# Performance work log

Measured on AMD Instinct MI355X. Metric: run time of the kernel, lower is better.

Reference implementation:

```python
import jax, jax.numpy as jnp
import numpy as np

INF = 1.0e15  # matches the TF module's 1e15 additive mask constant


def setup_inputs() -> dict:
    key = jax.random.key(0)
    kq, kk, kv, kp = jax.random.split(key, 4)
    B, S, D = 8, 4096, 64
    q = jax.random.normal(kq, (B, S, D), dtype=jnp.float32)
    k = jax.random.normal(kk, (B, S, D), dtype=jnp.float32)
    v = jax.random.normal(kv, (B, S, D), dtype=jnp.float32)
    # binary key-padding mask: 1 = masked. Broadcasts over seq_q.
    pad_mask = jax.random.randint(kp, (B, 1, S), 0, 2).astype(jnp.float32)
    # causal look-ahead mask: 1 above the diagonal (future positions masked)
    look_ahead_mask = (1.0 - jnp.tril(jnp.ones((S, S), dtype=jnp.float32)))
    return {"q": q, "k": k, "v": v, "pad_mask": pad_mask,
            "look_ahead_mask": look_ahead_mask}


def reference(q, k, v, pad_mask, look_ahead_mask):
    d_model = jnp.asarray(q.shape[2], dtype=q.dtype)
    # (B, Sq, Sk) score matrix, scaled
    score_logits = jnp.einsum("bqd,bkd->bqk", q, k) / jnp.sqrt(d_model)
    score_logits = score_logits + pad_mask * (-INF)          # broadcast (B,1,Sk)
    score_logits = score_logits + look_ahead_mask * (-INF)   # broadcast (Sq,Sk)
    attention_weight = jax.nn.softmax(score_logits, axis=-1)
    context_vector = jnp.einsum("bqk,bkd->bqd", attention_weight, v)
    return context_vector, attention_weight
```

## Files before the change

kernel.cpp:

```cpp
#include <hip/hip_runtime.h>

#define S_LEN 4096
#define D_DIM 64
#define NEG_BIG 1.0e15f
#define NC1 8
#define SSTAT (8 * 64 * NC1 * 64)
#define NPAD_OFF SSTAT
#define WS_FLOATS_NEEDED (NPAD_OFF + 16)
#define VSTRIDE 70

typedef __bf16 bf16_t;
typedef bf16_t bf16x8 __attribute__((ext_vector_type(8)));
typedef bf16_t bf16x4v __attribute__((ext_vector_type(4)));
typedef bf16_t bf16x2v __attribute__((ext_vector_type(2)));
typedef float f32x4v __attribute__((ext_vector_type(4)));

__global__ void sdpa_prep(const float* __restrict__ Pg, float* __restrict__ ws)
{
    __shared__ float red[16];
    const int b   = blockIdx.x;
    const int tid = threadIdx.x;

    float cnt = 0.f, first = (float)S_LEN;
    const float* pb = Pg + (size_t)b * S_LEN;
    for (int i = tid; i < S_LEN; i += 256) {
        float p = pb[i];
        cnt += 1.f - p;
        if (p == 0.f) first = fminf(first, (float)i);
    }
    #pragma unroll
    for (int off = 32; off >= 1; off >>= 1) {
        cnt += __shfl_down(cnt, off);
        first = fminf(first, __shfl_down(first, off));
    }
    const int w = tid >> 6, lane = tid & 63;
    if (lane == 0) { red[w] = cnt; red[8 + w] = first; }
    __syncthreads();
    if (tid == 0) {
        ws[NPAD_OFF + b]     = red[0] + red[1] + red[2] + red[3];
        ws[NPAD_OFF + 8 + b] = fminf(fminf(red[8], red[9]), fminf(red[10], red[11]));
    }
}

__global__ __launch_bounds__(256, 2)
void sdpa_stats(const float* __restrict__ Qg,
                const float* __restrict__ Kg,
                const float* __restrict__ Pg,
                float* __restrict__ ws,
                float* __restrict__ ctx,
                float* __restrict__ Wg)
{
    __shared__ __align__(16) bf16_t Ks[64][72];
    __shared__ float pads[64];

    const int tid  = threadIdx.x;
    const int w    = tid >> 6;
    const int lane = tid & 63;
    const int g    = lane >> 4;
    const int c    = lane & 15;
    const int gx   = blockIdx.x;
    const int b    = gx & 7;
    const int t    = gx >> 3;
    const int qt   = 63 - (t & 63);
    const int kc   = t >> 6;
    const int q0   = qt * 64;

    if (gx >= 2048) {
        f32x4v z = {0.f, 0.f, 0.f, 0.f};
        *(f32x4v*)(ctx + (size_t)(gx - 2048) * 1024 + tid * 4) = z;
    }

    const int firstNP = (int)ws[NPAD_OFF + 8 + b];

    if (q0 >= firstNP) {
        const f32x4v z = {0.f, 0.f, 0.f, 0.f};
        float* wrow = Wg + (size_t)b * S_LEN * S_LEN + (size_t)q0 * S_LEN;
        for (int fz = qt + 1 + kc; fz < 64; fz += 8) {
            float* wbase = wrow + fz * 64;
            #pragma unroll
            for (int i = 0; i < 4; ++i) {
                int f4 = i * 256 + tid;
                int r  = f4 >> 4;
                int c4 = (f4 & 15) * 4;
                __builtin_nontemporal_store(z, (f32x4v*)(wbase + (size_t)r * S_LEN + c4));
            }
        }
    }

    if (kc * 8 > qt) return;

    bf16x8 qa[2];
    {
        const float* qrow = Qg + ((size_t)b * S_LEN + q0 + 16 * w + c) * D_DIM;
        #pragma unroll
        for (int ks = 0; ks < 2; ++ks) {
            float4 a0 = *(const float4*)(qrow + ks * 32 + 8 * g);
            float4 a1 = *(const float4*)(qrow + ks * 32 + 8 * g + 4);
            qa[ks][0]=(bf16_t)a0.x; qa[ks][1]=(bf16_t)a0.y; qa[ks][2]=(bf16_t)a0.z; qa[ks][3]=(bf16_t)a0.w;
            qa[ks][4]=(bf16_t)a1.x; qa[ks][5]=(bf16_t)a1.y; qa[ks][6]=(bf16_t)a1.z; qa[ks][7]=(bf16_t)a1.w;
        }
    }

    float l[4] = {0.f, 0.f, 0.f, 0.f};
    const int qgBase = q0 + 16 * w + 4 * g;
    const int kend = min(kc * 8 + 8, qt + 1);

    for (int kt = kc * 8; kt < kend; ++kt) {
        const int k0 = kt * 64;
        {
            const float* src = Kg + ((size_t)b * S_LEN + k0) * D_DIM;
            #pragma unroll
            for (int i = 0; i < 4; ++i) {
                int f4 = i * 256 + tid;
                int r  = f4 >> 4;
                int c4 = (f4 & 15) * 4;
                float4 v4 = *(const float4*)(src + (size_t)f4 * 4);
                bf16x4v bv;
                bv[0]=(bf16_t)v4.x; bv[1]=(bf16_t)v4.y; bv[2]=(bf16_t)v4.z; bv[3]=(bf16_t)v4.w;
                *(bf16x4v*)&Ks[r][c4] = bv;
            }
            if (tid < 64) pads[tid] = Pg[(size_t)b * S_LEN + k0 + tid] * (-NEG_BIG);
        }
        __syncthreads();

        f32x4v sc[4];
        #pragma unroll
        for (int ct = 0; ct < 4; ++ct) {
            sc[ct] = (f32x4v){0.f, 0.f, 0.f, 0.f};
            #pragma unroll
            for (int ks = 0; ks < 2; ++ks) {
                bf16x8 kb = *(const bf16x8*)&Ks[ct * 16 + c][ks * 32 + 8 * g];
                sc[ct] = __builtin_amdgcn_mfma_f32_16x16x32_bf16(qa[ks], kb, sc[ct], 0, 0, 0);
            }
        }
        #pragma unroll
        for (int ct = 0; ct < 4; ++ct) {
            float pn  = pads[ct * 16 + c];
            int   kgi = k0 + ct * 16 + c;
            #pragma unroll
            for (int r = 0; r < 4; ++r) {
                float lg = sc[ct][r] * 0.125f + pn;
                if (kgi > qgBase + r) lg -= NEG_BIG;
                l[r] += __expf(lg);
            }
        }
        __syncthreads();
    }

    const size_t soff = ((size_t)((b * 64 + qt) * NC1 + kc)) * 64;
    #pragma unroll
    for (int r = 0; r < 4; ++r) {
        float s = l[r];
        s += __shfl_xor(s, 1);
        s += __shfl_xor(s, 2);
        s += __shfl_xor(s, 4);
        s += __shfl_xor(s, 8);
        l[r] = s;
    }
    if (c == 0) {
        #pragma unroll
        for (int r = 0; r < 4; ++r)
            ws[soff + 16 * w + 4 * g + r] = l[r];
    }
}

__global__ __launch_bounds__(256, 2)
void sdpa_wpv(const float* __restrict__ Qg,
              const float* __restrict__ Kg,
              const float* __restrict__ Vg,
              const float* __restrict__ Pg,
              float* __restrict__ Wg,
              float* __restrict__ ws,
              float* __restrict__ ctx)
{
    __shared__ __align__(16) bf16_t Ks[64][72];
    __shared__ __align__(16) bf16_t VT[64][VSTRIDE];
    __shared__ __align__(16) bf16_t Pf[64][72];
    __shared__ float pads[64];
    __shared__ float Lrow[64];

    const int tid  = threadIdx.x;
    const int w    = tid >> 6;
    const int lane = tid & 63;
    const int g    = lane >> 4;
    const int c    = lane & 15;
    const int gx   = blockIdx.x;
    const int b    = gx & 7;
    const int t    = gx >> 3;
    const int qt   = 63 - (t & 63);
    const int kc   = t >> 6;
    const int q0   = qt * 64;
    const int kstart = kc * 8;

    const float npadTot = ws[NPAD_OFF + b];
    const int   firstNP = (int)ws[NPAD_OFF + 8 + b];
    const bool  blockDeg = (q0 < firstNP);

    if (kstart > qt && !blockDeg) return;

    if (tid < 64) {
        int qrow = q0 + tid;
        float L;
        if (qrow < firstNP) {
            L = (float)(qrow + 1) + npadTot;
        } else {
            const float* sb = ws + (size_t)(b * 64 + qt) * NC1 * 64 + tid;
            L = 0.f;
            const int need = (qt >> 3) + 1;
            for (int i = 0; i < need; ++i) L += sb[(size_t)i * 64];
        }
        Lrow[tid] = 1.f / L;
    }
    __syncthreads();

    float* wchunk = Wg + (size_t)b * S_LEN * S_LEN + (size_t)q0 * S_LEN;

    bf16x8 qa[2];
    {
        const float* qrow = Qg + ((size_t)b * S_LEN + q0 + 16 * w + c) * D_DIM;
        #pragma unroll
        for (int ks = 0; ks < 2; ++ks) {
            float4 a0 = *(const float4*)(qrow + ks * 32 + 8 * g);
            float4 a1 = *(const float4*)(qrow + ks * 32 + 8 * g + 4);
            qa[ks][0]=(bf16_t)a0.x; qa[ks][1]=(bf16_t)a0.y; qa[ks][2]=(bf16_t)a0.z; qa[ks][3]=(bf16_t)a0.w;
            qa[ks][4]=(bf16_t)a1.x; qa[ks][5]=(bf16_t)a1.y; qa[ks][6]=(bf16_t)a1.z; qa[ks][7]=(bf16_t)a1.w;
        }
    }

    const int qgBase = q0 + 16 * w + 4 * g;
    float linv[4];
    #pragma unroll
    for (int r = 0; r < 4; ++r) linv[r] = Lrow[16 * w + 4 * g + r];

    f32x4v o[4];
    #pragma unroll
    for (int dt = 0; dt < 4; ++dt) o[dt] = (f32x4v){0.f, 0.f, 0.f, 0.f};

    const int kend2 = blockDeg ? (kstart + 8) : min(kstart + 8, qt + 1);

    for (int kt = kstart; kt < kend2; ++kt) {
        const int k0 = kt * 64;
        float* wbase = wchunk + k0;

        const float* ksrc = Kg + ((size_t)b * S_LEN + k0) * D_DIM;
        const float* vsrc = Vg + ((size_t)b * S_LEN + k0) * D_DIM;
        #pragma unroll
        for (int i = 0; i < 4; ++i) {
            int f4 = i * 256 + tid;
            int r  = f4 >> 4;
            int c4 = (f4 & 15) * 4;
            float4 kv = *(const float4*)(ksrc + (size_t)f4 * 4);
            bf16x4v bv;
            bv[0]=(bf16_t)kv.x; bv[1]=(bf16_t)kv.y; bv[2]=(bf16_t)kv.z; bv[3]=(bf16_t)kv.w;
            *(bf16x4v*)&Ks[r][c4] = bv;
            float4 vv = *(const float4*)(vsrc + (size_t)f4 * 4);
            VT[c4 + 0][r] = (bf16_t)vv.x;
            VT[c4 + 1][r] = (bf16_t)vv.y;
            VT[c4 + 2][r] = (bf16_t)vv.z;
            VT[c4 + 3][r] = (bf16_t)vv.w;
        }
        if (tid < 64) pads[tid] = Pg[(size_t)b * S_LEN + k0 + tid] * (-NEG_BIG);
        __syncthreads();

        f32x4v sc[4];
        #pragma unroll
        for (int ct = 0; ct < 4; ++ct) {
            sc[ct] = (f32x4v){0.f, 0.f, 0.f, 0.f};
            #pragma unroll
            for (int ks = 0; ks < 2; ++ks) {
                bf16x8 kb = *(const bf16x8*)&Ks[ct * 16 + c][ks * 32 + 8 * g];
                sc[ct] = __builtin_amdgcn_mfma_f32_16x16x32_bf16(qa[ks], kb, sc[ct], 0, 0, 0);
            }
        }
        if (!blockDeg) {
            #pragma unroll
            for (int ct = 0; ct < 4; ++ct) {
                float pn  = pads[ct * 16 + c];
                int   kgi = k0 + ct * 16 + c;
                #pragma unroll
                for (int r = 0; r < 4; ++r) {
                    float lg = sc[ct][r] * 0.125f + pn;
                    if (kgi > qgBase + r) lg -= NEG_BIG;
                    float wv = __expf(lg) * linv[r];
                    __builtin_nontemporal_store(wv,
                        wbase + (size_t)(16 * w + 4 * g + r) * S_LEN + ct * 16 + c);
                    Pf[16 * w + 4 * g + r][ct * 16 + c] = (bf16_t)wv;
                }
            }
        } else {
            #pragma unroll
            for (int ct = 0; ct < 4; ++ct) {
                float pn  = pads[ct * 16 + c];
                int   kgi = k0 + ct * 16 + c;
                #pragma unroll
                for (int r = 0; r < 4; ++r) {
                    float lg = sc[ct][r] * 0.125f + pn;
                    if (kgi > qgBase + r) lg -= NEG_BIG;
                    float wv = __expf(lg) * linv[r];
                    if (qgBase + r < firstNP)
                        wv = (kgi <= qgBase + r || pn == 0.f) ? linv[r] : 0.f;
                    __builtin_nontemporal_store(wv,
                        wbase + (size_t)(16 * w + 4 * g + r) * S_LEN + ct * 16 + c);
                    Pf[16 * w + 4 * g + r][ct * 16 + c] = (bf16_t)wv;
                }
            }
        }

        #pragma unroll
        for (int ks = 0; ks < 2; ++ks) {
            bf16x8 wa = *(const bf16x8*)&Pf[16 * w + c][ks * 32 + 8 * g];
            #pragma unroll
            for (int dt = 0; dt < 4; ++dt) {
                bf16x8 vb;
                #pragma unroll
                for (int p = 0; p < 4; ++p)
                    ((bf16x2v*)&vb)[p] = *(const bf16x2v*)&VT[dt * 16 + c][ks * 32 + 8 * g + 2 * p];
                o[dt] = __builtin_amdgcn_mfma_f32_16x16x32_bf16(wa, vb, o[dt], 0, 0, 0);
            }
        }
        __syncthreads();
    }

    #pragma unroll
    for (int dt = 0; dt < 4; ++dt)
        #pragma unroll
        for (int r = 0; r < 4; ++r)
            atomicAdd(&ctx[((size_t)b * S_LEN + (q0 + 16 * w + 4 * g + r)) * D_DIM + dt * 16 + c],
                      o[dt][r]);
}

__global__ __launch_bounds__(256, 2)
void sdpa_fused(const float* __restrict__ Qg,
                const float* __restrict__ Kg,
                const float* __restrict__ Vg,
                const float* __restrict__ Pg,
                float* __restrict__ Og,
                float* __restrict__ Wg)
{
    __shared__ __align__(16) bf16_t Qs[64][72];
    __shared__ __align__(16) bf16_t Ks[64][72];
    __shared__ __align__(16) bf16_t VT[64][72];
    __shared__ __align__(16) float  Wf[64][68];
    __shared__ float pads[64];
    __shared__ float red[4];
    __shared__ int   anyDeg;

    const int tid  = threadIdx.x;
    const int w    = tid >> 6;
    const int lane = tid & 63;
    const int g    = lane >> 4;
    const int c    = lane & 15;
    const int b    = blockIdx.x & 7;
    const int qt   = 63 - (blockIdx.x >> 3);
    const int q0   = qt * 64;

    if (tid == 0) anyDeg = 0;

    {
        const float* src = Qg + ((size_t)b * S_LEN + q0) * D_DIM;
        #pragma unroll
        for (int i = 0; i < 4; ++i) {
            int f4 = i * 256 + tid;
            int r  = f4 >> 4;
            int c4 = (f4 & 15) * 4;
            float4 v4 = *(const float4*)(src + (size_t)f4 * 4);
            bf16x4v bv;
            bv[0]=(bf16_t)v4.x; bv[1]=(bf16_t)v4.y; bv[2]=(bf16_t)v4.z; bv[3]=(bf16_t)v4.w;
            *(bf16x4v*)&Qs[r][c4] = bv;
        }
    }
    __syncthreads();

    bf16x8 qa[2];
    {
        int row = 16 * w + c;
        #pragma unroll
        for (int ks = 0; ks < 2; ++ks)
            qa[ks] = *(const bf16x8*)&Qs[row][ks * 32 + 8 * g];
    }

    float m[4], l[4];
    #pragma unroll
    for (int r = 0; r < 4; ++r) { m[r] = -INFINITY; l[r] = 0.f; }
    const int qgBase = q0 + 16 * w + 4 * g;

    for (int kt = 0; kt <= qt; ++kt) {
        const int k0 = kt * 64;
        {
            const float* src = Kg + ((size_t)b * S_LEN + k0) * D_DIM;
            #pragma unroll
            for (int i = 0; i < 4; ++i) {
                int f4 = i * 256 + tid;
                int r  = f4 >> 4;
                int c4 = (f4 & 15) * 4;
                float4 v4 = *(const float4*)(src + (size_t)f4 * 4);
                bf16x4v bv;
                bv[0]=(bf16_t)v4.x; bv[1]=(bf16_t)v4.y; bv[2]=(bf16_t)v4.z; bv[3]=(bf16_t)v4.w;
                *(bf16x4v*)&Ks[r][c4] = bv;
            }
            if (tid < 64) pads[tid] = Pg[(size_t)b * S_LEN + k0 + tid] * (-NEG_BIG);
        }
        __syncthreads();

        f32x4v sc[4];
        #pragma unroll
        for (int ct = 0; ct < 4; ++ct) {
            sc[ct] = (f32x4v){0.f, 0.f, 0.f, 0.f};
            #pragma unroll
            for (int ks = 0; ks < 2; ++ks) {
                bf16x8 kb = *(const bf16x8*)&Ks[ct * 16 + c][ks * 32 + 8 * g];
                sc[ct] = __builtin_amdgcn_mfma_f32_16x16x32_bf16(qa[ks], kb, sc[ct], 0, 0, 0);
            }
        }
        float l4[4][4];
        #pragma unroll
        for (int ct = 0; ct < 4; ++ct) {
            float pn  = pads[ct * 16 + c];
            int   kgi = k0 + ct * 16 + c;
            #pragma unroll
            for (int r = 0; r < 4; ++r) {
                float lg = sc[ct][r] * 0.125f + pn;
                if (kgi > qgBase + r) lg -= NEG_BIG;
                l4[ct][r] = lg;
            }
        }
        #pragma unroll
        for (int r = 0; r < 4; ++r) {
            float tm = fmaxf(fmaxf(l4[0][r], l4[1][r]), fmaxf(l4[2][r], l4[3][r]));
            tm = fmaxf(tm, __shfl_xor(tm, 1));
            tm = fmaxf(tm, __shfl_xor(tm, 2));
            tm = fmaxf(tm, __shfl_xor(tm, 4));
            tm = fmaxf(tm, __shfl_xor(tm, 8));
            float mnew = fmaxf(m[r], tm);
            float s = __expf(l4[0][r] - mnew) + __expf(l4[1][r] - mnew)
                    + __expf(l4[2][r] - mnew) + __expf(l4[3][r] - mnew);
            s += __shfl_xor(s, 1);
            s += __shfl_xor(s, 2);
            s += __shfl_xor(s, 4);
            s += __shfl_xor(s, 8);
            l[r] = l[r] * __expf(m[r] - mnew) + s;
            m[r] = mnew;
        }
        __syncthreads();
    }

    {
        float cnt = 0.f;
        const float* pb = Pg + (size_t)b * S_LEN;
        for (int i = tid; i < S_LEN; i += 256) cnt += 1.f - pb[i];
        #pragma unroll
        for (int off = 32; off >= 1; off >>= 1) cnt += __shfl_down(cnt, off);
        if (lane == 0) red[w] = cnt;
    }
    __syncthreads();
    {
        float nonpad = red[0] + red[1] + red[2] + red[3];
        bool deg = false;
        #pragma unroll
        for (int r = 0; r < 4; ++r)
            if (m[r] < -1.0e14f) { l[r] += nonpad; deg = true; }
        if (deg) anyDeg = 1;
    }
    __syncthreads();
    const bool blockDeg = (anyDeg != 0);
    float linv[4];
    #pragma unroll
    for (int r = 0; r < 4; ++r) linv[r] = 1.f / l[r];

    f32x4v o[4];
    #pragma unroll
    for (int dt = 0; dt < 4; ++dt) o[dt] = (f32x4v){0.f, 0.f, 0.f, 0.f};

    for (int kt = 0; kt < 64; ++kt) {
        const int k0 = kt * 64;
        float* wbase = Wg + (size_t)b * S_LEN * S_LEN + (size_t)q0 * S_LEN + k0;

        if (kt <= qt || blockDeg) {
            const float* ksrc = Kg + ((size_t)b * S_LEN + k0) * D_DIM;
            const float* vsrc = Vg + ((size_t)b * S_LEN + k0) * D_DIM;
            #pragma unroll
            for (int i = 0; i < 4; ++i) {
                int f4 = i * 256 + tid;
                int r  = f4 >> 4;
                int c4 = (f4 & 15) * 4;
                float4 kv = *(const float4*)(ksrc + (size_t)f4 * 4);
                bf16x4v bv;
                bv[0]=(bf16_t)kv.x; bv[1]=(bf16_t)kv.y; bv[2]=(bf16_t)kv.z; bv[3]=(bf16_t)kv.w;
                *(bf16x4v*)&Ks[r][c4] = bv;
                float4 vv = *(const float4*)(vsrc + (size_t)f4 * 4);
                VT[c4 + 0][r] = (bf16_t)vv.x;
                VT[c4 + 1][r] = (bf16_t)vv.y;
                VT[c4 + 2][r] = (bf16_t)vv.z;
                VT[c4 + 3][r] = (bf16_t)vv.w;
            }
            if (tid < 64) pads[tid] = Pg[(size_t)b * S_LEN + k0 + tid] * (-NEG_BIG);
            __syncthreads();

            f32x4v sc[4];
            #pragma unroll
            for (int ct = 0; ct < 4; ++ct) {
                sc[ct] = (f32x4v){0.f, 0.f, 0.f, 0.f};
                #pragma unroll
                for (int ks = 0; ks < 2; ++ks) {
                    bf16x8 kb = *(const bf16x8*)&Ks[ct * 16 + c][ks * 32 + 8 * g];
                    sc[ct] = __builtin_amdgcn_mfma_f32_16x16x32_bf16(qa[ks], kb, sc[ct], 0, 0, 0);
                }
            }
            #pragma unroll
            for (int ct = 0; ct < 4; ++ct) {
                float pn  = pads[ct * 16 + c];
                int   kgi = k0 + ct * 16 + c;
                #pragma unroll
                for (int r = 0; r < 4; ++r) {
                    float lg = sc[ct][r] * 0.125f + pn;
                    if (kgi > qgBase + r) lg -= NEG_BIG;
                    float wv = __expf(lg - m[r]) * linv[r];
                    Wf[16 * w + 4 * g + r][ct * 16 + c] = wv;
                }
            }
            __syncthreads();

            #pragma unroll
            for (int i = 0; i < 4; ++i) {
                int f4 = i * 256 + tid;
                int r  = f4 >> 4;
                int c4 = (f4 & 15) * 4;
                float4 wv = *(const float4*)&Wf[r][c4];
                *(float4*)(wbase + (size_t)r * S_LEN + c4) = wv;
            }

            #pragma unroll
            for (int ks = 0; ks < 2; ++ks) {
                float4 f0 = *(const float4*)&Wf[16 * w + c][ks * 32 + 8 * g];
                float4 f1 = *(const float4*)&Wf[16 * w + c][ks * 32 + 8 * g + 4];
                bf16x8 wa;
                wa[0]=(bf16_t)f0.x; wa[1]=(bf16_t)f0.y; wa[2]=(bf16_t)f0.z; wa[3]=(bf16_t)f0.w;
                wa[4]=(bf16_t)f1.x; wa[5]=(bf16_t)f1.y; wa[6]=(bf16_t)f1.z; wa[7]=(bf16_t)f1.w;
                #pragma unroll
                for (int dt = 0; dt < 4; ++dt) {
                    bf16x8 vb = *(const bf16x8*)&VT[dt * 16 + c][ks * 32 + 8 * g];
                    o[dt] = __builtin_amdgcn_mfma_f32_16x16x32_bf16(wa, vb, o[dt], 0, 0, 0);
                }
            }
            __syncthreads();
        } else {
            const float4 z = {0.f, 0.f, 0.f, 0.f};
            #pragma unroll
            for (int i = 0; i < 4; ++i) {
                int f4 = i * 256 + tid;
                int r  = f4 >> 4;
                int c4 = (f4 & 15) * 4;
                *(float4*)(wbase + (size_t)r * S_LEN + c4) = z;
            }
        }
    }

    #pragma unroll
    for (int dt = 0; dt < 4; ++dt)
        #pragma unroll
        for (int r = 0; r < 4; ++r)
            Og[((size_t)b * S_LEN + (q0 + 16 * w + 4 * g + r)) * D_DIM + dt * 16 + c] = o[dt][r];
}

extern "C" void kernel_launch(void* const* d_in, const int* in_sizes, int n_in,
                              void* d_out, int out_size, void* d_ws, size_t ws_size,
                              hipStream_t stream) {
    const float* q   = (const float*)d_in[0];
    const float* k   = (const float*)d_in[1];
    const float* v   = (const float*)d_in[2];
    const float* pad = (const float*)d_in[3];

    float* out  = (float*)d_out;
    float* ctx  = out;
    float* attw = out + (size_t)8 * 4096 * 64;
    float* ws   = (float*)d_ws;

    if (ws_size >= (size_t)WS_FLOATS_NEEDED * 4) {
        hipLaunchKernelGGL(sdpa_prep,  dim3(8),    dim3(256), 0, stream, pad, ws);
        hipLaunchKernelGGL(sdpa_stats, dim3(4096), dim3(256), 0, stream, q, k, pad, ws, ctx, attw);
        hipLaunchKernelGGL(sdpa_wpv,   dim3(4096), dim3(256), 0, stream, q, k, v, pad, attw, ws, ctx);
    } else {
        hipLaunchKernelGGL(sdpa_fused, dim3(512), dim3(256), 0, stream, q, k, v, pad, ctx, attw);
    }
}
```

Baseline: 171.2 us.

## Process two 64-row query tiles per block to reuse K/V tiles

Each block in the stats and weight/PV kernels now covers 128 query rows (two 64-row sub-tiles) instead of 64, and the grid is halved. Each K/V tile loaded into shared memory and converted to bf16 is used for twice as many MFMAs, which cuts global K/V reads and barrier overhead per unit of work. The cost is more registers and shared memory per block (larger Pf and Lrow buffers, doubled accumulators). Causal work also balances more coarsely, since the upper sub-tile may run tiles that are fully masked for the lower one.

```diff
diff --git a/kernel.cpp b/kernel.cpp
--- a/kernel.cpp
+++ b/kernel.cpp
@@ -61,49 +61,56 @@
     const int gx   = blockIdx.x;
     const int b    = gx & 7;
     const int t    = gx >> 3;
-    const int qt   = 63 - (t & 63);
-    const int kc   = t >> 6;
-    const int q0   = qt * 64;
-
-    if (gx >= 2048) {
+    const int qtt  = 31 - (t & 31);
+    const int kc   = t >> 5;
+    const int qt_hi = 2 * qtt + 1;
+    const int q0   = qtt * 128;
+
+    {
         f32x4v z = {0.f, 0.f, 0.f, 0.f};
-        *(f32x4v*)(ctx + (size_t)(gx - 2048) * 1024 + tid * 4) = z;
+        *(f32x4v*)(ctx + (size_t)gx * 1024 + tid * 4) = z;
     }
 
     const int firstNP = (int)ws[NPAD_OFF + 8 + b];
 
-    if (q0 >= firstNP) {
-        const f32x4v z = {0.f, 0.f, 0.f, 0.f};
-        float* wrow = Wg + (size_t)b * S_LEN * S_LEN + (size_t)q0 * S_LEN;
-        for (int fz = qt + 1 + kc; fz < 64; fz += 8) {
-            float* wbase = wrow + fz * 64;
-            #pragma unroll
-            for (int i = 0; i < 4; ++i) {
-                int f4 = i * 256 + tid;
-                int r  = f4 >> 4;
-                int c4 = (f4 & 15) * 4;
-                __builtin_nontemporal_store(z, (f32x4v*)(wbase + (size_t)r * S_LEN + c4));
-            }
-        }
-    }
-
-    if (kc * 8 > qt) return;
-
-    bf16x8 qa[2];
-    {
-        const float* qrow = Qg + ((size_t)b * S_LEN + q0 + 16 * w + c) * D_DIM;
+    #pragma unroll
+    for (int h = 0; h < 2; ++h) {
+        const int qts = 2 * qtt + h;
+        const int q0s = qts * 64;
+        if (q0s >= firstNP) {
+            const f32x4v z = {0.f, 0.f, 0.f, 0.f};
+            float* wrow = Wg + (size_t)b * S_LEN * S_LEN + (size_t)q0s * S_LEN;
+            for (int fz = qts + 1 + kc; fz < 64; fz += 8) {
+                float* wbase = wrow + fz * 64;
+                #pragma unroll
+                for (int i = 0; i < 4; ++i) {
+                    int f4 = i * 256 + tid;
+                    int r  = f4 >> 4;
+                    int c4 = (f4 & 15) * 4;
+                    __builtin_nontemporal_store(z, (f32x4v*)(wbase + (size_t)r * S_LEN + c4));
+                }
+            }
+        }
+    }
+
+    if (kc * 8 > qt_hi) return;
+
+    bf16x8 qa[2][2];
+    #pragma unroll
+    for (int h = 0; h < 2; ++h) {
+        const float* qrow = Qg + ((size_t)b * S_LEN + q0 + 64 * h + 16 * w + c) * D_DIM;
         #pragma unroll
         for (int ks = 0; ks < 2; ++ks) {
             float4 a0 = *(const float4*)(qrow + ks * 32 + 8 * g);
             float4 a1 = *(const float4*)(qrow + ks * 32 + 8 * g + 4);
-            qa[ks][0]=(bf16_t)a0.x; qa[ks][1]=(bf16_t)a0.y; qa[ks][2]=(bf16_t)a0.z; qa[ks][3]=(bf16_t)a0.w;
-            qa[ks][4]=(bf16_t)a1.x; qa[ks][5]=(bf16_t)a1.y; qa[ks][6]=(bf16_t)a1.z; qa[ks][7]=(bf16_t)a1.w;
-        }
-    }
-
-    float l[4] = {0.f, 0.f, 0.f, 0.f};
-    const int qgBase = q0 + 16 * w + 4 * g;
-    const int kend = min(kc * 8 + 8, qt + 1);
+            qa[h][ks][0]=(bf16_t)a0.x; qa[h][ks][1]=(bf16_t)a0.y; qa[h][ks][2]=(bf16_t)a0.z; qa[h][ks][3]=(bf16_t)a0.w;
+            qa[h][ks][4]=(bf16_t)a1.x; qa[h][ks][5]=(bf16_t)a1.y; qa[h][ks][6]=(bf16_t)a1.z; qa[h][ks][7]=(bf16_t)a1.w;
+        }
+    }
+
+    float l[2][4] = {{0.f,0.f,0.f,0.f},{0.f,0.f,0.f,0.f}};
+    const int qgB0 = q0 + 16 * w + 4 * g;
+    const int kend = min(kc * 8 + 8, qt_hi + 1);
 
     for (int kt = kc * 8; kt < kend; ++kt) {
         const int k0 = kt * 64;
@@ -123,44 +130,53 @@
         }
         __syncthreads();
 
-        f32x4v sc[4];
+        f32x4v sc[2][4];
         #pragma unroll
         for (int ct = 0; ct < 4; ++ct) {
-            sc[ct] = (f32x4v){0.f, 0.f, 0.f, 0.f};
+            sc[0][ct] = (f32x4v){0.f, 0.f, 0.f, 0.f};
+            sc[1][ct] = (f32x4v){0.f, 0.f, 0.f, 0.f};
             #pragma unroll
             for (int ks = 0; ks < 2; ++ks) {
                 bf16x8 kb = *(const bf16x8*)&Ks[ct * 16 + c][ks * 32 + 8 * g];
-                sc[ct] = __builtin_amdgcn_mfma_f32_16x16x32_bf16(qa[ks], kb, sc[ct], 0, 0, 0);
-            }
-        }
-        #pragma unroll
-        for (int ct = 0; ct < 4; ++ct) {
-            float pn  = pads[ct * 16 + c];
-            int   kgi = k0 + ct * 16 + c;
-            #pragma unroll
-            for (int r = 0; r < 4; ++r) {
-                float lg = sc[ct][r] * 0.125f + pn;
-                if (kgi > qgBase + r) lg -= NEG_BIG;
-                l[r] += __expf(lg);
+                sc[0][ct] = __builtin_amdgcn_mfma_f32_16x16x32_bf16(qa[0][ks], kb, sc[0][ct], 0, 0, 0);
+                sc[1][ct] = __builtin_amdgcn_mfma_f32_16x16x32_bf16(qa[1][ks], kb, sc[1][ct], 0, 0, 0);
+            }
+        }
+        #pragma unroll
+        for (int h = 0; h < 2; ++h) {
+            const int qgB = qgB0 + 64 * h;
+            #pragma unroll
+            for (int ct = 0; ct < 4; ++ct) {
+                float pn  = pads[ct * 16 + c];
+                int   kgi = k0 + ct * 16 + c;
+                #pragma unroll
+                for (int r = 0; r < 4; ++r) {
+                    float lg = sc[h][ct][r] * 0.125f + pn;
+                    if (kgi > qgB + r) lg -= NEG_BIG;
+                    l[h][r] += __expf(lg);
+                }
             }
         }
         __syncthreads();
     }
 
-    const size_t soff = ((size_t)((b * 64 + qt) * NC1 + kc)) * 64;
-    #pragma unroll
-    for (int r = 0; r < 4; ++r) {
-        float s = l[r];
-        s += __shfl_xor(s, 1);
-        s += __shfl_xor(s, 2);
-        s += __shfl_xor(s, 4);
-        s += __shfl_xor(s, 8);
-        l[r] = s;
-    }
-    if (c == 0) {
-        #pragma unroll
-        for (int r = 0; r < 4; ++r)
-            ws[soff + 16 * w + 4 * g + r] = l[r];
+    #pragma unroll
+    for (int h = 0; h < 2; ++h) {
+        const size_t soff = ((size_t)((b * 64 + 2 * qtt + h) * NC1 + kc)) * 64;
+        #pragma unroll
+        for (int r = 0; r < 4; ++r) {
+            float s = l[h][r];
+            s += __shfl_xor(s, 1);
+            s += __shfl_xor(s, 2);
+            s += __shfl_xor(s, 4);
+            s += __shfl_xor(s, 8);
+            l[h][r] = s;
+        }
+        if (c == 0) {
+            #pragma unroll
+            for (int r = 0; r < 4; ++r)
+                ws[soff + 16 * w + 4 * g + r] = l[h][r];
+        }
     }
 }
 
@@ -175,9 +191,9 @@
 {
     __shared__ __align__(16) bf16_t Ks[64][72];
     __shared__ __align__(16) bf16_t VT[64][VSTRIDE];
-    __shared__ __align__(16) bf16_t Pf[64][72];
+    __shared__ __align__(16) bf16_t Pf[128][72];
     __shared__ float pads[64];
-    __shared__ float Lrow[64];
+    __shared__ float Lrow[128];
 
     const int tid  = threadIdx.x;
     const int w    = tid >> 6;
@@ -187,26 +203,28 @@
     const int gx   = blockIdx.x;
     const int b    = gx & 7;
     const int t    = gx >> 3;
-    const int qt   = 63 - (t & 63);
-    const int kc   = t >> 6;
-    const int q0   = qt * 64;
+    const int qtt  = 31 - (t & 31);
+    const int kc   = t >> 5;
+    const int qt_hi = 2 * qtt + 1;
+    const int q0   = qtt * 128;
     const int kstart = kc * 8;
 
     const float npadTot = ws[NPAD_OFF + b];
     const int   firstNP = (int)ws[NPAD_OFF + 8 + b];
     const bool  blockDeg = (q0 < firstNP);
 
-    if (kstart > qt && !blockDeg) return;
-
-    if (tid < 64) {
-        int qrow = q0 + tid;
+    if (kstart > qt_hi && !blockDeg) return;
+
+    if (tid < 128) {
+        const int row = q0 + tid;
         float L;
-        if (qrow < firstNP) {
-            L = (float)(qrow + 1) + npadTot;
+        if (row < firstNP) {
+            L = (float)(row + 1) + npadTot;
         } else {
-            const float* sb = ws + (size_t)(b * 64 + qt) * NC1 * 64 + tid;
+            const int qtr = row >> 6;
+            const float* sb = ws + (size_t)(b * 64 + qtr) * NC1 * 64 + (row & 63);
             L = 0.f;
-            const int need = (qt >> 3) + 1;
+            const int need = (qtr >> 3) + 1;
             for (int i = 0; i < need; ++i) L += sb[(size_t)i * 64];
         }
         Lrow[tid] = 1.f / L;
@@ -215,28 +233,35 @@
 
     float* wchunk = Wg + (size_t)b * S_LEN * S_LEN + (size_t)q0 * S_LEN;
 
-    bf16x8 qa[2];
-    {
-        const float* qrow = Qg + ((size_t)b * S_LEN + q0 + 16 * w + c) * D_DIM;
+    bf16x8 qa[2][2];
+    #pragma unroll
+    for (int h = 0; h < 2; ++h) {
+        const float* qrow = Qg + ((size_t)b * S_LEN + q0 + 64 * h + 16 * w + c) * D_DIM;
         #pragma unroll
         for (int ks = 0; ks < 2; ++ks) {
             float4 a0 = *(const float4*)(qrow + ks * 32 + 8 * g);
             float4 a1 = *(const float4*)(qrow + ks * 32 + 8 * g + 4);
-            qa[ks][0]=(bf16_t)a0.x; qa[ks][1]=(bf16_t)a0.y; qa[ks][2]=(bf16_t)a0.z; qa[ks][3]=(bf16_t)a0.w;
-            qa[ks][4]=(bf16_t)a1.x; qa[ks][5]=(bf16_t)a1.y; qa[ks][6]=(bf16_t)a1.z; qa[ks][7]=(bf16_t)a1.w;
-        }
-    }
-
-    const int qgBase = q0 + 16 * w + 4 * g;
-    float linv[4];
-    #pragma unroll
-    for (int r = 0; r < 4; ++r) linv[r] = Lrow[16 * w + 4 * g + r];
-
-    f32x4v o[4];
-    #pragma unroll
-    for (int dt = 0; dt < 4; ++dt) o[dt] = (f32x4v){0.f, 0.f, 0.f, 0.f};
-
-    const int kend2 = blockDeg ? (kstart + 8) : min(kstart + 8, qt + 1);
+            qa[h][ks][0]=(bf16_t)a0.x; qa[h][ks][1]=(bf16_t)a0.y; qa[h][ks][2]=(bf16_t)a0.z; qa[h][ks][3]=(bf16_t)a0.w;
+            qa[h][ks][4]=(bf16_t)a1.x; qa[h][ks][5]=(bf16_t)a1.y; qa[h][ks][6]=(bf16_t)a1.z; qa[h][ks][7]=(bf16_t)a1.w;
+        }
+    }
+
+    const int qgB0 = q0 + 16 * w + 4 * g;
+    float linv[2][4];
+    #pragma unroll
+    for (int h = 0; h < 2; ++h)
+        #pragma unroll
+        for (int r = 0; r < 4; ++r)
+            linv[h][r] = Lrow[64 * h + 16 * w + 4 * g + r];
+
+    f32x4v o[2][4];
+    #pragma unroll
+    for (int h = 0; h < 2; ++h)
+        #pragma unroll
+        for (int dt = 0; dt < 4; ++dt)
+            o[h][dt] = (f32x4v){0.f, 0.f, 0.f, 0.f};
+
+    const int kend2 = blockDeg ? (kstart + 8) : min(kstart + 8, qt_hi + 1);
 
     for (int kt = kstart; kt < kend2; ++kt) {
         const int k0 = kt * 64;
@@ -262,71 +287,80 @@
         if (tid < 64) pads[tid] = Pg[(size_t)b * S_LEN + k0 + tid] * (-NEG_BIG);
         __syncthreads();
 
-        f32x4v sc[4];
-        #pragma unroll
-        for (int ct = 0; ct < 4; ++ct) {
-            sc[ct] = (f32x4v){0.f, 0.f, 0.f, 0.f};
-            #pragma unroll
-            for (int ks = 0; ks < 2; ++ks) {
-                bf16x8 kb = *(const bf16x8*)&Ks[ct * 16 + c][ks * 32 + 8 * g];
-                sc[ct] = __builtin_amdgcn_mfma_f32_16x16x32_bf16(qa[ks], kb, sc[ct], 0, 0, 0);
-            }
-        }
-        if (!blockDeg) {
+        #pragma unroll
+        for (int h = 0; h < 2; ++h) {
+            f32x4v sc[4];
             #pragma unroll
             for (int ct = 0; ct < 4; ++ct) {
-                float pn  = pads[ct * 16 + c];
-                int   kgi = k0 + ct * 16 + c;
-                #pragma unroll
-                for (int r = 0; r < 4; ++r) {
-                    float lg = sc[ct][r] * 0.125f + pn;
-                    if (kgi > qgBase + r) lg -= NEG_BIG;
-                    float wv = __expf(lg) * linv[r];
-                    __builtin_nontemporal_store(wv,
-                        wbase + (size_t)(16 * w + 4 * g + r) * S_LEN + ct * 16 + c);
-                    Pf[16 * w + 4 * g + r][ct * 16 + c] = (bf16_t)wv;
-                }
-            }
-        } else {
-            #pragma unroll
-            for (int ct = 0; ct < 4; ++ct) {
-                float pn  = pads[ct * 16 + c];
-                int   kgi = k0 + ct * 16 + c;
-                #pragma unroll
-                for (int r = 0; r < 4; ++r) {
-                    float lg = sc[ct][r] * 0.125f + pn;
-                    if (kgi > qgBase + r) lg -= NEG_BIG;
-                    float wv = __expf(lg) * linv[r];
-                    if (qgBase + r < firstNP)
-                        wv = (kgi <= qgBase + r || pn == 0.f) ? linv[r] : 0.f;
-                    __builtin_nontemporal_store(wv,
-                        wbase + (size_t)(16 * w + 4 * g + r) * S_LEN + ct * 16 + c);
-                    Pf[16 * w + 4 * g + r][ct * 16 + c] = (bf16_t)wv;
+                sc[ct] = (f32x4v){0.f, 0.f, 0.f, 0.f};
+                #pragma unroll
+                for (int ks = 0; ks < 2; ++ks) {
+                    bf16x8 kb = *(const bf16x8*)&Ks[ct * 16 + c][ks * 32 + 8 * g];
+                    sc[ct] = __builtin_amdgcn_mfma_f32_16x16x32_bf16(qa[h][ks], kb, sc[ct], 0, 0, 0);
+                }
+            }
+            const int qgB = qgB0 + 64 * h;
+            const int prow = 64 * h + 16 * w + 4 * g;
+            if (!blockDeg) {
+                #pragma unroll
+                for (int ct = 0; ct < 4; ++ct) {
+                    float pn  = pads[ct * 16 + c];
+                    int   kgi = k0 + ct * 16 + c;
+                    #pragma unroll
+                    for (int r = 0; r < 4; ++r) {
+                        float lg = sc[ct][r] * 0.125f + pn;
+                        if (kgi > qgB + r) lg -= NEG_BIG;
+                        float wv = __expf(lg) * linv[h][r];
+                        __builtin_nontemporal_store(wv,
+                            wbase + (size_t)(prow + r) * S_LEN + ct * 16 + c);
+                        Pf[prow + r][ct * 16 + c] = (bf16_t)wv;
+                    }
+                }
+            } else {
+                #pragma unroll
+                for (int ct = 0; ct < 4; ++ct) {
+                    float pn  = pads[ct * 16 + c];
+                    int   kgi = k0 + ct * 16 + c;
+                    #pragma unroll
+                    for (int r = 0; r < 4; ++r) {
+                        float lg = sc[ct][r] * 0.125f + pn;
+                        if (kgi > qgB + r) lg -= NEG_BIG;
+                        float wv = __expf(lg) * linv[h][r];
+                        if (qgB + r < firstNP)
+                            wv = (kgi <= qgB + r || pn == 0.f) ? linv[h][r] : 0.f;
+                        __builtin_nontemporal_store(wv,
+                            wbase + (size_t)(prow + r) * S_LEN + ct * 16 + c);
+                        Pf[prow + r][ct * 16 + c] = (bf16_t)wv;
+                    }
                 }
             }
         }
 
         #pragma unroll
         for (int ks = 0; ks < 2; ++ks) {
-            bf16x8 wa = *(const bf16x8*)&Pf[16 * w + c][ks * 32 + 8 * g];
+            bf16x8 wa0 = *(const bf16x8*)&Pf[16 * w + c][ks * 32 + 8 * g];
+            bf16x8 wa1 = *(const bf16x8*)&Pf[64 + 16 * w + c][ks * 32 + 8 * g];
             #pragma unroll
             for (int dt = 0; dt < 4; ++dt) {
                 bf16x8 vb;
                 #pragma unroll
                 for (int p = 0; p < 4; ++p)
                     ((bf16x2v*)&vb)[p] = *(const bf16x2v*)&VT[dt * 16 + c][ks * 32 + 8 * g + 2 * p];
-                o[dt] = __builtin_amdgcn_mfma_f32_16x16x32_bf16(wa, vb, o[dt], 0, 0, 0);
+                o[0][dt] = __builtin_amdgcn_mfma_f32_16x16x32_bf16(wa0, vb, o[0][dt], 0, 0, 0);
+                o[1][dt] = __builtin_amdgcn_mfma_f32_16x16x32_bf16(wa1, vb, o[1][dt], 0, 0, 0);
             }
         }
         __syncthreads();
     }
 
     #pragma unroll
-    for (int dt = 0; dt < 4; ++dt)
-        #pragma unroll
-        for (int r = 0; r < 4; ++r)
-            atomicAdd(&ctx[((size_t)b * S_LEN + (q0 + 16 * w + 4 * g + r)) * D_DIM + dt * 16 + c],
-                      o[dt][r]);
+    for (int h = 0; h < 2; ++h)
+        #pragma unroll
+        for (int dt = 0; dt < 4; ++dt)
+            #pragma unroll
+            for (int r = 0; r < 4; ++r)
+                atomicAdd(&ctx[((size_t)b * S_LEN + (q0 + 64 * h + 16 * w + 4 * g + r)) * D_DIM + dt * 16 + c],
+                          o[h][dt][r]);
 }
 
 __global__ __launch_bounds__(256, 2)
@@ -577,8 +611,8 @@
 
     if (ws_size >= (size_t)WS_FLOATS_NEEDED * 4) {
         hipLaunchKernelGGL(sdpa_prep,  dim3(8),    dim3(256), 0, stream, pad, ws);
-        hipLaunchKernelGGL(sdpa_stats, dim3(4096), dim3(256), 0, stream, q, k, pad, ws, ctx, attw);
-        hipLaunchKernelGGL(sdpa_wpv,   dim3(4096), dim3(256), 0, stream, q, k, v, pad, attw, ws, ctx);
+        hipLaunchKernelGGL(sdpa_stats, dim3(2048), dim3(256), 0, stream, q, k, pad, ws, ctx, attw);
+        hipLaunchKernelGGL(sdpa_wpv,   dim3(2048), dim3(256), 0, stream, q, k, v, pad, attw, ws, ctx);
     } else {
         hipLaunchKernelGGL(sdpa_fused, dim3(512), dim3(256), 0, stream, q, k, v, pad, ctx, attw);
     }
```

Measured after the change: 193.1 us. 12.8% more time.
